# Optimization experiments

Measured on AMD Instinct MI355X. Metric: run time of the kernel, lower is better.

## Reference

```python
import jax, jax.numpy as jnp
import numpy as np

B, N, DIM, H, DH, P = 4, 4096, 256, 8, 64, 2
INNER = H * DH  # 512


def setup_inputs() -> dict:
    key = jax.random.key(0)
    ks = jax.random.split(key, 10)
    w = lambda k, shape: jax.random.normal(k, shape, dtype=jnp.float32) * 0.02
    return dict(
        x=jax.random.normal(ks[0], (B, N, DIM), dtype=jnp.float32),
        prev_x=jax.random.normal(ks[1], (B, N, DIM), dtype=jnp.float32),
        ln_q_g=jnp.ones((2 * DIM,), jnp.float32), ln_q_b=jnp.zeros((2 * DIM,), jnp.float32),
        ln_k_g=jnp.ones((DIM,), jnp.float32), ln_k_b=jnp.zeros((DIM,), jnp.float32),
        ln_v_g=jnp.ones((DIM,), jnp.float32), ln_v_b=jnp.zeros((DIM,), jnp.float32),
        Wq=w(ks[2], (2 * DIM, INNER)),            # to_q, bias=False
        Wk=w(ks[3], (DIM, INNER)), bk=jnp.zeros((INNER,), jnp.float32),
        Wv=w(ks[4], (DIM, INNER)), bv=jnp.zeros((INNER,), jnp.float32),
        Woff=w(ks[5], (H * P, INNER)),            # 1x1 conv == linear over channels
        boff=jax.random.uniform(ks[6], (H * P,), jnp.float32, -1.0, 1.0),
        Wout=w(ks[7], (DIM, INNER)), bout=jnp.zeros((DIM,), jnp.float32),
    )


def _ln(x, g, b):
    m = x.mean(-1, keepdims=True)
    v = ((x - m) ** 2).mean(-1, keepdims=True)
    return (x - m) * jax.lax.rsqrt(v + 1e-5) * g + b


def reference(x, prev_x, ln_q_g, ln_q_b, ln_k_g, ln_k_b, ln_v_g, ln_v_b,
              Wq, Wk, bk, Wv, bv, Woff, boff, Wout, bout):
    scale = DH ** -0.5
    # queries from cat(x, prev_x) along feature dim
    q = _ln(jnp.concatenate([x, prev_x], axis=-1), ln_q_g, ln_q_b) @ Wq  # (B,N,INNER)
    # learned per-head, per-point offsets (1x1 conv over channels)
    offsets = (q @ Woff.T + boff).reshape(B, N, H, P).transpose(0, 2, 3, 1)  # (B,H,P,N)
    # K/V from cat(x, prev_x) along batch dim -> KV length 2N per (b,h)
    kv = jnp.concatenate([x, prev_x], axis=0)  # (2B,N,DIM)
    k = (_ln(kv, ln_k_g, ln_k_b) @ Wk + bk).reshape(2, B, N, H, DH).transpose(1, 3, 4, 0, 2).reshape(B, H, DH, 2 * N)
    v = (_ln(kv, ln_v_g, ln_v_b) @ Wv + bv).reshape(2, B, N, H, DH).transpose(1, 3, 4, 0, 2).reshape(B, H, DH, 2 * N)
    # sampling positions: pos + offset, clamped, truncated to int (matches torch .long())
    pos = jnp.arange(N, dtype=jnp.float32)
    samp = jnp.clip(pos[None, None, None, :] + offsets, 0, 2 * N - 1).astype(jnp.int32)  # (B,H,P,N)
    idx = samp.transpose(0, 1, 3, 2)[:, :, None, :, :]  # (B,H,1,N,P)
    k_s = jnp.take_along_axis(k[:, :, :, None, :], idx, axis=-1)  # (B,H,DH,N,P)
    v_s = jnp.take_along_axis(v[:, :, :, None, :], idx, axis=-1)  # (B,H,DH,N,P)
    qh = q.reshape(B, N, H, DH).transpose(0, 2, 1, 3) * scale     # (B,H,N,DH)
    sim = jnp.einsum('bhnd,bhdnp->bhnp', qh, k_s)                  # (B,H,N,P)
    attn = jax.nn.softmax(sim, axis=-1)
    out = jnp.einsum('bhnp,bhdnp->bhnd', attn, v_s)                # (B,H,N,DH)
    out = out.transpose(0, 2, 1, 3).reshape(B, N, INNER) @ Wout.T + bout  # (B,N,DIM)
    return out, offsets
```

## Files before the change

### kernel.cpp

```cpp
#include <hip/hip_runtime.h>
#include <hip/hip_bf16.h>
#include <math.h>

#define B_    4
#define N_    4096
#define DIM_  256
#define H_    8
#define DH_   64
#define P_    2
#define INNER_ 512
#define BN_   (B_ * N_)
#define KVR_  (2 * BN_)

typedef short v8s  __attribute__((ext_vector_type(8)));
typedef short v4s  __attribute__((ext_vector_type(4)));
typedef float v4f  __attribute__((ext_vector_type(4)));

__device__ __forceinline__ short f2b(float x) {
    __hip_bfloat16 h = __float2bfloat16(x);
    return *reinterpret_cast<short*>(&h);
}
__device__ __forceinline__ float b2f(short s) {
    __hip_bfloat16 h = *reinterpret_cast<__hip_bfloat16*>(&s);
    return __bfloat162float(h);
}

__device__ __forceinline__ void async16(const void* g, void* l) {
    __builtin_amdgcn_global_load_lds(
        (const __attribute__((address_space(1))) void*)g,
        (__attribute__((address_space(3))) void*)l, 16, 0, 0);
}

__device__ __forceinline__ void storeRow(float* p, float4 f0, float4 f1, float4 f2, float4 f3) {
    ((float4*)p)[0] = f0; ((float4*)p)[1] = f1; ((float4*)p)[2] = f2; ((float4*)p)[3] = f3;
}
__device__ __forceinline__ void storeRow(__hip_bfloat16* p, float4 f0, float4 f1, float4 f2, float4 f3) {
    v8s o0, o1;
    o0[0]=f2b(f0.x); o0[1]=f2b(f0.y); o0[2]=f2b(f0.z); o0[3]=f2b(f0.w);
    o0[4]=f2b(f1.x); o0[5]=f2b(f1.y); o0[6]=f2b(f1.z); o0[7]=f2b(f1.w);
    o1[0]=f2b(f2.x); o1[1]=f2b(f2.y); o1[2]=f2b(f2.z); o1[3]=f2b(f2.w);
    o1[4]=f2b(f3.x); o1[5]=f2b(f3.y); o1[6]=f2b(f3.z); o1[7]=f2b(f3.w);
    ((v8s*)p)[0] = o0; ((v8s*)p)[1] = o1;
}

__global__ __launch_bounds__(256) void prep_all(
    const float* __restrict__ Wq, const float* __restrict__ gq, const float* __restrict__ betaq,
    const float* __restrict__ Wk, const float* __restrict__ gk, const float* __restrict__ betak,
    const float* __restrict__ bk,
    const float* __restrict__ Wv, const float* __restrict__ gv, const float* __restrict__ betav,
    const float* __restrict__ bv,
    const float* __restrict__ Woff, const float* __restrict__ Wout,
    short* __restrict__ Wq2t, float* __restrict__ bq2,
    short* __restrict__ Wkvt, float* __restrict__ bkv,
    float* __restrict__ Wcomb, float* __restrict__ braw, short* __restrict__ Woutb) {
    __shared__ float sm[272];
    const int bid = blockIdx.x, t = threadIdx.x;

    if (bid < 1536) {
        const float *W, *g, *beta, *bias_in;
        short* Wt; float* b2; int K, n; float scale;
        if (bid < 512)       { W=Wq; g=gq; beta=betaq; bias_in=nullptr; Wt=Wq2t; b2=bq2; K=512; n=bid;        scale=0.125f; }
        else if (bid < 1024) { W=Wk; g=gk; beta=betak; bias_in=bk; Wt=Wkvt;           b2=bkv;       K=256; n=bid-512;  scale=1.f; }
        else                 { W=Wv; g=gv; beta=betav; bias_in=bv; Wt=Wkvt+512*256;   b2=bkv+512;   K=256; n=bid-1024; scale=1.f; }
        float partial = 0.f;
        for (int k = t; k < K; k += 256) {
            float w = W[k * 512 + n];
            Wt[(size_t)n * K + k] = f2b(scale * g[k] * w);
            partial += beta[k] * w;
        }
        sm[t] = partial;
        __syncthreads();
        for (int s = 128; s > 0; s >>= 1) {
            if (t < s) sm[t] += sm[t + s];
            __syncthreads();
        }
        if (t == 0) b2[n] = scale * ((bias_in ? bias_in[n] : 0.f) + sm[0]);
    } else if (bid < 2048) {
        const int k = bid - 1536;
        const int hp = t & 15, jg = t >> 4;
        float p = 0.f;
        for (int j = jg; j < INNER_; j += 16)
            p += Wq[k * INNER_ + j] * Woff[hp * INNER_ + j];
        sm[jg * 17 + hp] = p;
        __syncthreads();
        if (t < 16) {
            float s = 0.f;
            for (int i = 0; i < 16; i++) s += sm[i * 17 + t];
            Wcomb[k * 16 + t] = gq[k] * s;
            braw[k * 16 + t]  = betaq[k] * s;
        }
    } else {
        const int i0 = (bid - 2048) * 1024 + t * 4;
        float4 f = *(const float4*)(Wout + i0);
        v4s o;
        o[0] = f2b(f.x); o[1] = f2b(f.y); o[2] = f2b(f.z); o[3] = f2b(f.w);
        *(v4s*)(Woutb + i0) = o;
    }
}

__global__ void bcomb_sum(const float* __restrict__ braw, const float* __restrict__ boff,
                          float* __restrict__ bcomb) {
    __shared__ float sm[272];
    int t = threadIdx.x;
    int hp = t & 15, kg = t >> 4;
    float p = 0.f;
    for (int k = kg; k < 512; k += 16) p += braw[k * 16 + hp];
    sm[kg * 17 + hp] = p;
    __syncthreads();
    if (t < 16) {
        float s = 0.f;
        for (int i = 0; i < 16; i++) s += sm[i * 17 + t];
        bcomb[t] = s + boff[t];
    }
}

__global__ __launch_bounds__(256) void norm_fused_kernel(
    const float* __restrict__ x, const float* __restrict__ p,
    const float* __restrict__ Wcomb, const float* __restrict__ bcomb,
    short* __restrict__ Aq, short* __restrict__ Akv,
    float* __restrict__ out_off, int* __restrict__ idx) {
    const int lane = threadIdx.x & 63;
    const int wv   = threadIdx.x >> 6;
    const int m0   = (blockIdx.x * 4 + wv) * 4;
    const int k8   = lane * 8;

    float4 w[8][4];
#pragma unroll
    for (int i = 0; i < 8; i++) {
        const float4* wr = (const float4*)(Wcomb + (size_t)(k8 + i) * 16);
#pragma unroll
        for (int j = 0; j < 4; j++) w[i][j] = wr[j];
    }
    const float bc = bcomb[lane & 15];

    const float* srcb = (lane < 32) ? (x + k8) : (p + k8 - DIM_);

    float4 u0 = ((const float4*)(srcb + (size_t)m0 * DIM_))[0];
    float4 u1 = ((const float4*)(srcb + (size_t)m0 * DIM_))[1];

#pragma unroll
    for (int r = 0; r < 4; r++) {
        const int m = m0 + r;
        float4 n0, n1;
        if (r < 3) {
            n0 = ((const float4*)(srcb + (size_t)(m + 1) * DIM_))[0];
            n1 = ((const float4*)(srcb + (size_t)(m + 1) * DIM_))[1];
        }
        float uv[8] = { u0.x, u0.y, u0.z, u0.w, u1.x, u1.y, u1.z, u1.w };

        float s = 0.f, q2 = 0.f;
#pragma unroll
        for (int i = 0; i < 8; i++) { s += uv[i]; q2 += uv[i] * uv[i]; }
#pragma unroll
        for (int d = 1; d <= 16; d <<= 1) {
            s  += __shfl_xor(s, d);
            q2 += __shfl_xor(q2, d);
        }
        float mean_h = s * (1.f / 256.f);
        float var_h  = q2 * (1.f / 256.f) - mean_h * mean_h;
        float rstd_h = rsqrtf(var_h + 1e-5f);
        float sf  = s  + __shfl_xor(s, 32);
        float q2f = q2 + __shfl_xor(q2, 32);
        float mean_q = sf * (1.f / 512.f);
        float var_q  = q2f * (1.f / 512.f) - mean_q * mean_q;
        float rstd_q = rsqrtf(var_q + 1e-5f);

        v8s okv;
#pragma unroll
        for (int i = 0; i < 8; i++) okv[i] = f2b((uv[i] - mean_h) * rstd_h);
        short* akvdst = Akv + ((lane < 32) ? ((size_t)m * DIM_ + k8)
                                           : ((size_t)(BN_ + m) * DIM_ + k8 - DIM_));
        *(v8s*)akvdst = okv;

        float nv[8];
        v8s oq;
#pragma unroll
        for (int i = 0; i < 8; i++) { nv[i] = (uv[i] - mean_q) * rstd_q; oq[i] = f2b(nv[i]); }
        *(v8s*)(Aq + (size_t)m * INNER_ + k8) = oq;

        float acc[16];
#pragma unroll
        for (int h = 0; h < 16; h++) acc[h] = 0.f;
#pragma unroll
        for (int i = 0; i < 8; i++) {
            float nvi = nv[i];
            acc[0]  += nvi * w[i][0].x;  acc[1]  += nvi * w[i][0].y;
            acc[2]  += nvi * w[i][0].z;  acc[3]  += nvi * w[i][0].w;
            acc[4]  += nvi * w[i][1].x;  acc[5]  += nvi * w[i][1].y;
            acc[6]  += nvi * w[i][1].z;  acc[7]  += nvi * w[i][1].w;
            acc[8]  += nvi * w[i][2].x;  acc[9]  += nvi * w[i][2].y;
            acc[10] += nvi * w[i][2].z;  acc[11] += nvi * w[i][2].w;
            acc[12] += nvi * w[i][3].x;  acc[13] += nvi * w[i][3].y;
            acc[14] += nvi * w[i][3].z;  acc[15] += nvi * w[i][3].w;
        }
        float a8[8];
#pragma unroll
        for (int j = 0; j < 8; j++) {
            float lo = acc[2 * j] + __shfl_xor(acc[2 * j], 1);
            float hi = acc[2 * j + 1] + __shfl_xor(acc[2 * j + 1], 1);
            a8[j] = (lane & 1) ? hi : lo;
        }
        float a4[4];
#pragma unroll
        for (int j = 0; j < 4; j++) {
            float lo = a8[2 * j] + __shfl_xor(a8[2 * j], 2);
            float hi = a8[2 * j + 1] + __shfl_xor(a8[2 * j + 1], 2);
            a4[j] = (lane & 2) ? hi : lo;
        }
        float a2[2];
#pragma unroll
        for (int j = 0; j < 2; j++) {
            float lo = a4[2 * j] + __shfl_xor(a4[2 * j], 4);
            float hi = a4[2 * j + 1] + __shfl_xor(a4[2 * j + 1], 4);
            a2[j] = (lane & 4) ? hi : lo;
        }
        float l1 = a2[0] + __shfl_xor(a2[0], 8);
        float h1 = a2[1] + __shfl_xor(a2[1], 8);
        float a1 = (lane & 8) ? h1 : l1;
        a1 += __shfl_xor(a1, 16);
        a1 += __shfl_xor(a1, 32);

        if (lane < 16) {
            float off = a1 + bc;
            int b = m >> 12, n = m & (N_ - 1);
            int h = lane >> 1, pp = lane & 1;
            out_off[(size_t)((b * H_ + h) * P_ + pp) * N_ + n] = off;
            float f = fminf(fmaxf((float)n + off, 0.f), (float)(2 * N_ - 1));
            idx[((size_t)(b * H_ + h) * N_ + n) * P_ + pp] = (int)f;
        }
        u0 = n0; u1 = n1;
    }
}

template <typename OT>
__device__ __forceinline__ void gemm_body(
    short* smem, const short* __restrict__ A, const short* __restrict__ Bt,
    const float* __restrict__ bias, OT* __restrict__ C, int N, int K, int nx, int lin) {
    short* As = smem;
    short* Bs = smem + 128 * 64;
    const int tid  = threadIdx.x;
    const int lane = tid & 63, w = tid >> 6;
    const int wr = w >> 1, wc = w & 1;
    const int lm = lane & 15, g = lane >> 4;

    const int x8 = lin & 7, t = lin >> 3;
    const int bx = t % nx, by = (t / nx) * 8 + x8;
    const int row0 = by * 128, col0 = bx * 128;

    const short* pa[4];
    const short* pb[4];
#pragma unroll
    for (int r = 0; r < 4; r++) {
        int s   = tid + 256 * r;
        int row = s >> 3, kcs = s & 7;
        int kg  = kcs ^ (row & 7);
        pa[r] = A  + (size_t)(row0 + row) * K + kg * 8;
        pb[r] = Bt + (size_t)(col0 + row) * K + kg * 8;
    }

    v4f acc[4][4];
#pragma unroll
    for (int i = 0; i < 4; i++)
#pragma unroll
        for (int j = 0; j < 4; j++) acc[i][j] = (v4f){0.f, 0.f, 0.f, 0.f};

    for (int k0 = 0; k0 < K; k0 += 64) {
        __syncthreads();
#pragma unroll
        for (int r = 0; r < 4; r++) {
            int s = tid + 256 * r;
            async16(pa[r] + k0, (char*)As + s * 16);
            async16(pb[r] + k0, (char*)Bs + s * 16);
        }
        __syncthreads();
#pragma unroll
        for (int ks = 0; ks < 2; ks++) {
            v8s af[4], bf[4];
#pragma unroll
            for (int i = 0; i < 4; i++) {
                int m   = wr * 64 + i * 16 + lm;
                int sch = m * 8 + ((ks * 4 + g) ^ (m & 7));
                af[i] = *(const v8s*)(As + sch * 8);
            }
#pragma unroll
            for (int j = 0; j < 4; j++) {
                int n   = wc * 64 + j * 16 + lm;
                int sch = n * 8 + ((ks * 4 + g) ^ (n & 7));
                bf[j] = *(const v8s*)(Bs + sch * 8);
            }
#pragma unroll
            for (int i = 0; i < 4; i++)
#pragma unroll
                for (int j = 0; j < 4; j++)
                    acc[i][j] = __builtin_amdgcn_mfma_f32_16x16x32_bf16(af[i], bf[j], acc[i][j], 0, 0, 0);
        }
    }

#pragma unroll
    for (int j = 0; j < 4; j++) {
        int gc = col0 + wc * 64 + j * 16 + lm;
        float bj = bias ? bias[gc] : 0.f;
#pragma unroll
        for (int i = 0; i < 4; i++)
#pragma unroll
            for (int r = 0; r < 4; r++) acc[i][j][r] += bj;
    }

    __syncthreads();
    float* ep = (float*)smem + w * (16 * 68);
#pragma unroll
    for (int i = 0; i < 4; i++) {
#pragma unroll
        for (int j = 0; j < 4; j++)
#pragma unroll
            for (int r = 0; r < 4; r++)
                ep[(g * 4 + r) * 68 + j * 16 + lm] = acc[i][j][r];
        asm volatile("s_waitcnt lgkmcnt(0)" ::: "memory");
        int rr = lane >> 2, cb = (lane & 3) * 16;
        float4 f0 = *(float4*)(ep + rr * 68 + cb + 0);
        float4 f1 = *(float4*)(ep + rr * 68 + cb + 4);
        float4 f2 = *(float4*)(ep + rr * 68 + cb + 8);
        float4 f3 = *(float4*)(ep + rr * 68 + cb + 12);
        asm volatile("s_waitcnt lgkmcnt(0)" ::: "memory");
        int grow = row0 + wr * 64 + i * 16 + rr;
        int gcol = col0 + wc * 64 + cb;
        storeRow(&C[(size_t)grow * N + gcol], f0, f1, f2, f3);
    }
}

#define ATILE_ (256 * 64)

__global__ __launch_bounds__(512, 2) void gemm_qkv_256(
    const short* __restrict__ Aqp, const short* __restrict__ Wq2t,
    const float* __restrict__ bq2, __hip_bfloat16* __restrict__ qb,
    const short* __restrict__ Akvp, const short* __restrict__ Wkvt,
    const float* __restrict__ bkv, __hip_bfloat16* __restrict__ kvproj) {
    __shared__ short smem[4 * ATILE_];

    const short* A; const short* Bt; const float* bias; __hip_bfloat16* C;
    int N, K, NT, nxs, nwg, lin;
    if ((int)blockIdx.x < 128) {
        A = Aqp;  Bt = Wq2t; bias = bq2; C = qb;
        N = 512;  K = 512; NT = 8; nxs = 1; nwg = 128; lin = blockIdx.x;
    } else {
        A = Akvp; Bt = Wkvt; bias = bkv; C = kvproj;
        N = 1024; K = 256; NT = 4; nxs = 2; nwg = 512; lin = blockIdx.x - 128;
    }

    const int tid  = threadIdx.x;
    const int lane = tid & 63, w = tid >> 6;
    const int wr = w >> 2, wc = w & 3;
    const int lm = lane & 15, g = lane >> 4;

    const int wg = (lin & 7) * (nwg >> 3) + (lin >> 3);
    const int bx = wg & ((1 << nxs) - 1), by = wg >> nxs;
    const int row0 = by << 8, col0 = bx << 8;

    short* As0 = smem;
    short* Bs0 = smem + 2 * ATILE_;

    const int kg = ((tid & 7) ^ ((tid >> 3) & 7)) << 3;
    const short* gA = A  + (size_t)(row0 + (tid >> 3)) * K + kg;
    const short* gB = Bt + (size_t)(col0 + (tid >> 3)) * K + kg;

    auto stageA = [&](int buf, int k0) {
        char* lp = (char*)(As0 + buf * ATILE_);
#pragma unroll
        for (int r = 0; r < 4; r++)
            async16(gA + (size_t)r * 64 * K + k0, lp + r * 8192 + tid * 16);
    };
    auto stageB = [&](int buf, int k0) {
        char* lp = (char*)(Bs0 + buf * ATILE_);
#pragma unroll
        for (int r = 0; r < 4; r++)
            async16(gB + (size_t)r * 64 * K + k0, lp + r * 8192 + tid * 16);
    };

    v4f acc[8][4];
#pragma unroll
    for (int i = 0; i < 8; i++)
#pragma unroll
        for (int j = 0; j < 4; j++) acc[i][j] = (v4f){0.f, 0.f, 0.f, 0.f};

    float bj[4];
#pragma unroll
    for (int jj = 0; jj < 4; jj++) bj[jj] = bias[col0 + wc * 64 + jj * 16 + lm];

    v8s aLo[4][2], aHi[4][2], bF[4][2];

    auto RD_A = [&](const short* base, int half, v8s (*dst)[2]) {
#pragma unroll
        for (int i = 0; i < 4; i++) {
            const int m = wr * 128 + half * 64 + i * 16 + lm;
#pragma unroll
            for (int ks = 0; ks < 2; ks++)
                dst[i][ks] = *(const v8s*)(base + m * 64 + (((ks << 2) | g) ^ (m & 7)) * 8);
        }
    };
    auto RD_B = [&](const short* base) {
#pragma unroll
        for (int j = 0; j < 4; j++) {
            const int n = wc * 64 + j * 16 + lm;
#pragma unroll
            for (int ks = 0; ks < 2; ks++)
                bF[j][ks] = *(const v8s*)(base + n * 64 + (((ks << 2) | g) ^ (n & 7)) * 8);
        }
    };
    auto MFMA_H = [&](int half, v8s (*af)[2]) {
        __builtin_amdgcn_s_setprio(1);
#pragma unroll
        for (int i = 0; i < 4; i++)
#pragma unroll
            for (int j = 0; j < 4; j++) {
                acc[half*4+i][j] = __builtin_amdgcn_mfma_f32_16x16x32_bf16(af[i][0], bF[j][0], acc[half*4+i][j], 0, 0, 0);
                acc[half*4+i][j] = __builtin_amdgcn_mfma_f32_16x16x32_bf16(af[i][1], bF[j][1], acc[half*4+i][j], 0, 0, 0);
            }
        __builtin_amdgcn_s_setprio(0);
    };

    stageB(0, 0); stageA(0, 0);
    stageB(1, 64); stageA(1, 64);
    asm volatile("s_waitcnt vmcnt(8)" ::: "memory");
    __builtin_amdgcn_s_barrier();
    asm volatile("" ::: "memory");

    for (int T = 0; T < NT; ++T) {
        const int cur = T & 1;
        const short* as = As0 + cur * ATILE_;
        const short* bs = Bs0 + cur * ATILE_;
        const bool s2 = (T + 2 < NT);
        const int k2 = (T + 2) << 6;

        RD_B(bs);
        RD_A(as, 0, aLo);
        asm volatile("s_waitcnt lgkmcnt(0)" ::: "memory");
        __builtin_amdgcn_s_barrier();
        if (s2) stageB(cur, k2);
        MFMA_H(0, aLo);
        RD_A(as, 1, aHi);
        asm volatile("s_waitcnt lgkmcnt(0)" ::: "memory");
        __builtin_amdgcn_s_barrier();
        if (s2) stageA(cur, k2);
        MFMA_H(1, aHi);
        if (s2)              asm volatile("s_waitcnt vmcnt(8)" ::: "memory");
        else if (T + 1 < NT) asm volatile("s_waitcnt vmcnt(0)" ::: "memory");
        __builtin_amdgcn_s_barrier();
        asm volatile("" ::: "memory");
    }

    float* ep = (float*)smem + w * (16 * 68);
#pragma unroll
    for (int ii = 0; ii < 8; ii++) {
#pragma unroll
        for (int jj = 0; jj < 4; jj++)
#pragma unroll
            for (int r = 0; r < 4; r++)
                ep[(g * 4 + r) * 68 + jj * 16 + lm] = acc[ii][jj][r] + bj[jj];
        asm volatile("s_waitcnt lgkmcnt(0)" ::: "memory");
        const int rr = lane >> 2, cb = (lane & 3) * 16;
        float4 f0 = *(float4*)(ep + rr * 68 + cb + 0);
        float4 f1 = *(float4*)(ep + rr * 68 + cb + 4);
        float4 f2 = *(float4*)(ep + rr * 68 + cb + 8);
        float4 f3 = *(float4*)(ep + rr * 68 + cb + 12);
        asm volatile("s_waitcnt lgkmcnt(0)" ::: "memory");
        const int grow = row0 + wr * 128 + ii * 16 + rr;
        const int gcol = col0 + wc * 64 + cb;
        storeRow(&C[(size_t)grow * N + gcol], f0, f1, f2, f3);
    }
}

__global__ __launch_bounds__(256) void gemm_out(
    const short* __restrict__ A, const short* __restrict__ Bt,
    const float* __restrict__ bias, float* __restrict__ C) {
    __shared__ short smem[2 * 128 * 64];
    const int lin = blockIdx.y * gridDim.x + blockIdx.x;
    gemm_body<float>(smem, A, Bt, bias, C, 256, 512, 2, lin);
}

__global__ __launch_bounds__(256) void attn_kernel(
    const short* __restrict__ qb, const short* __restrict__ kvproj,
    const int* __restrict__ idx, short* __restrict__ attnout) {
    const int lane = threadIdx.x & 63;
    const int wv   = threadIdx.x >> 6;
    const int s    = lane >> 4, c = lane & 15;
    const int n = blockIdx.x * 16 + wv * 4 + s;
    const int h = blockIdx.y, b = blockIdx.z;
    const int m = b * N_ + n;

    v4s qv = *(const v4s*)(qb + (size_t)m * INNER_ + h * DH_ + c * 4);

    const int* ip = idx + ((size_t)(b * H_ + h) * N_ + n) * P_;
    int j0 = ip[0], j1 = ip[1];
    int r0 = b * N_ + j0 + ((j0 >= N_) ? (BN_ - N_) : 0);
    int r1 = b * N_ + j1 + ((j1 >= N_) ? (BN_ - N_) : 0);
    const short* k0p = kvproj + (size_t)r0 * 1024 + h * DH_ + c * 4;
    const short* k1p = kvproj + (size_t)r1 * 1024 + h * DH_ + c * 4;
    v4s k0 = *(const v4s*)k0p, v0 = *(const v4s*)(k0p + 512);
    v4s k1 = *(const v4s*)k1p, v1 = *(const v4s*)(k1p + 512);

    float q0 = b2f(qv[0]), q1 = b2f(qv[1]), q2 = b2f(qv[2]), q3 = b2f(qv[3]);
    float s0 = q0 * b2f(k0[0]) + q1 * b2f(k0[1]) + q2 * b2f(k0[2]) + q3 * b2f(k0[3]);
    float s1 = q0 * b2f(k1[0]) + q1 * b2f(k1[1]) + q2 * b2f(k1[2]) + q3 * b2f(k1[3]);
#pragma unroll
    for (int d = 1; d <= 8; d <<= 1) {
        s0 += __shfl_xor(s0, d);
        s1 += __shfl_xor(s1, d);
    }
    float mx = fmaxf(s0, s1);
    float e0 = __expf(s0 - mx), e1 = __expf(s1 - mx);
    float inv = 1.f / (e0 + e1);
    v4s o;
#pragma unroll
    for (int i = 0; i < 4; i++)
        o[i] = f2b((e0 * b2f(v0[i]) + e1 * b2f(v1[i])) * inv);
    *(v4s*)(attnout + (size_t)m * INNER_ + h * DH_ + c * 4) = o;
}

extern "C" void kernel_launch(void* const* d_in, const int* in_sizes, int n_in,
                              void* d_out, int out_size, void* d_ws, size_t ws_size,
                              hipStream_t stream) {
    (void)in_sizes; (void)n_in; (void)out_size; (void)ws_size;

    const float* x      = (const float*)d_in[0];
    const float* prevx  = (const float*)d_in[1];
    const float* ln_q_g = (const float*)d_in[2];
    const float* ln_q_b = (const float*)d_in[3];
    const float* ln_k_g = (const float*)d_in[4];
    const float* ln_k_b = (const float*)d_in[5];
    const float* ln_v_g = (const float*)d_in[6];
    const float* ln_v_b = (const float*)d_in[7];
    const float* Wq     = (const float*)d_in[8];
    const float* Wk     = (const float*)d_in[9];
    const float* bk     = (const float*)d_in[10];
    const float* Wv     = (const float*)d_in[11];
    const float* bv     = (const float*)d_in[12];
    const float* Woff   = (const float*)d_in[13];
    const float* boff   = (const float*)d_in[14];
    const float* Wout   = (const float*)d_in[15];
    const float* bout   = (const float*)d_in[16];

    char* cur = (char*)d_ws;
    auto alloc = [&](size_t bytes) { char* p = cur; cur += (bytes + 255) & ~(size_t)255; return p; };
    short* Aq      = (short*)alloc((size_t)BN_ * INNER_ * 2);
    short* Akv     = (short*)alloc((size_t)KVR_ * DIM_ * 2);
    short* qb      = (short*)alloc((size_t)BN_ * INNER_ * 2);
    short* kvproj  = (short*)alloc((size_t)KVR_ * 1024 * 2);
    short* attnout = (short*)alloc((size_t)BN_ * INNER_ * 2);
    short* Wq2t    = (short*)alloc(512 * 512 * 2);
    short* Wkvt    = (short*)alloc(1024 * 256 * 2);
    short* Woutb   = (short*)alloc(256 * 512 * 2);
    float* bq2     = (float*)alloc(512 * 4);
    float* bkv     = (float*)alloc(1024 * 4);
    float* Wcomb   = (float*)alloc(512 * 16 * 4);
    float* braw    = (float*)alloc(512 * 16 * 4);
    float* bcomb   = (float*)alloc(16 * 4);
    int*   idxb    = (int*)alloc((size_t)BN_ * 16 * 4);

    float* out_main = (float*)d_out;
    float* out_off  = out_main + (size_t)BN_ * DIM_;

    prep_all<<<2176, 256, 0, stream>>>(Wq, ln_q_g, ln_q_b,
                                       Wk, ln_k_g, ln_k_b, bk,
                                       Wv, ln_v_g, ln_v_b, bv,
                                       Woff, Wout,
                                       Wq2t, bq2, Wkvt, bkv, Wcomb, braw, Woutb);
    bcomb_sum<<<1, 256, 0, stream>>>(braw, boff, bcomb);

    norm_fused_kernel<<<BN_ / 16, 256, 0, stream>>>(x, prevx, Wcomb, bcomb,
                                                    Aq, Akv, out_off, idxb);

    gemm_qkv_256<<<640, 512, 0, stream>>>(Aq, Wq2t, bq2, (__hip_bfloat16*)qb,
                                          Akv, Wkvt, bkv, (__hip_bfloat16*)kvproj);

    dim3 ga(N_ / 16, H_, B_);
    attn_kernel<<<ga, 256, 0, stream>>>(qb, kvproj, idxb, attnout);

    gemm_out<<<dim3(2, 128), 256, 0, stream>>>(attnout, Woutb, bout, out_main);
}
```

Before: 216.4 us.

## Store Q/K/V head-major and fold bias reduction into norm kernel

The QKV GEMM epilogue now writes Q, K and V in a head-major layout ([h][row][64]), with V in a separate plane. This makes the attention kernel's per-head gathers touch contiguous 128-byte rows instead of strided 2KB rows. The separate single-block bcomb_sum launch is removed. Each norm block now recomputes the 16 offset biases redundantly from braw, which saves a launch but adds per-block reduction work.

```diff
diff --git a/kernel.cpp b/kernel.cpp
--- a/kernel.cpp
+++ b/kernel.cpp
@@ -11,6 +11,7 @@
 #define INNER_ 512
 #define BN_   (B_ * N_)
 #define KVR_  (2 * BN_)
+#define VOFF_ ((size_t)H_ * KVR_ * DH_)
 
 typedef short v8s  __attribute__((ext_vector_type(8)));
 typedef short v4s  __attribute__((ext_vector_type(4)));
@@ -34,7 +35,7 @@
 __device__ __forceinline__ void storeRow(float* p, float4 f0, float4 f1, float4 f2, float4 f3) {
     ((float4*)p)[0] = f0; ((float4*)p)[1] = f1; ((float4*)p)[2] = f2; ((float4*)p)[3] = f3;
 }
-__device__ __forceinline__ void storeRow(__hip_bfloat16* p, float4 f0, float4 f1, float4 f2, float4 f3) {
+__device__ __forceinline__ void storeRowS(short* p, float4 f0, float4 f1, float4 f2, float4 f3) {
     v8s o0, o1;
     o0[0]=f2b(f0.x); o0[1]=f2b(f0.y); o0[2]=f2b(f0.z); o0[3]=f2b(f0.w);
     o0[4]=f2b(f1.x); o0[5]=f2b(f1.y); o0[6]=f2b(f1.z); o0[7]=f2b(f1.w);
@@ -98,32 +99,35 @@
     }
 }
 
-__global__ void bcomb_sum(const float* __restrict__ braw, const float* __restrict__ boff,
-                          float* __restrict__ bcomb) {
-    __shared__ float sm[272];
-    int t = threadIdx.x;
-    int hp = t & 15, kg = t >> 4;
-    float p = 0.f;
-    for (int k = kg; k < 512; k += 16) p += braw[k * 16 + hp];
-    sm[kg * 17 + hp] = p;
-    __syncthreads();
-    if (t < 16) {
-        float s = 0.f;
-        for (int i = 0; i < 16; i++) s += sm[i * 17 + t];
-        bcomb[t] = s + boff[t];
-    }
-}
-
 __global__ __launch_bounds__(256) void norm_fused_kernel(
     const float* __restrict__ x, const float* __restrict__ p,
-    const float* __restrict__ Wcomb, const float* __restrict__ bcomb,
+    const float* __restrict__ Wcomb, const float* __restrict__ braw,
+    const float* __restrict__ boff,
     short* __restrict__ Aq, short* __restrict__ Akv,
     float* __restrict__ out_off, int* __restrict__ idx) {
+    __shared__ float smr[272];
+    const int t    = threadIdx.x;
     const int lane = threadIdx.x & 63;
     const int wv   = threadIdx.x >> 6;
     const int m0   = (blockIdx.x * 4 + wv) * 4;
     const int k8   = lane * 8;
 
+    {
+        const int hp = t & 15, kg = t >> 4;
+        float pp = 0.f;
+        for (int k = kg; k < 512; k += 16) pp += braw[k * 16 + hp];
+        smr[kg * 17 + hp] = pp;
+    }
+    __syncthreads();
+    if (t < 16) {
+        float s = 0.f;
+#pragma unroll
+        for (int i = 0; i < 16; i++) s += smr[i * 17 + t];
+        smr[256 + t] = s + boff[t];
+    }
+    __syncthreads();
+    const float bc = smr[256 + (lane & 15)];
+
     float4 w[8][4];
 #pragma unroll
     for (int i = 0; i < 8; i++) {
@@ -131,7 +135,6 @@
 #pragma unroll
         for (int j = 0; j < 4; j++) w[i][j] = wr[j];
     }
-    const float bc = bcomb[lane & 15];
 
     const float* srcb = (lane < 32) ? (x + k8) : (p + k8 - DIM_);
 
@@ -332,19 +335,20 @@
 
 __global__ __launch_bounds__(512, 2) void gemm_qkv_256(
     const short* __restrict__ Aqp, const short* __restrict__ Wq2t,
-    const float* __restrict__ bq2, __hip_bfloat16* __restrict__ qb,
+    const float* __restrict__ bq2, short* __restrict__ qbh,
     const short* __restrict__ Akvp, const short* __restrict__ Wkvt,
-    const float* __restrict__ bkv, __hip_bfloat16* __restrict__ kvproj) {
+    const float* __restrict__ bkv, short* __restrict__ khv) {
     __shared__ short smem[4 * ATILE_];
 
-    const short* A; const short* Bt; const float* bias; __hip_bfloat16* C;
-    int N, K, NT, nxs, nwg, lin;
+    const short* A; const short* Bt; const float* bias; short* C;
+    int K, NT, nxs, nwg, lin;
+    bool isQ;
     if ((int)blockIdx.x < 128) {
-        A = Aqp;  Bt = Wq2t; bias = bq2; C = qb;
-        N = 512;  K = 512; NT = 8; nxs = 1; nwg = 128; lin = blockIdx.x;
+        A = Aqp;  Bt = Wq2t; bias = bq2; C = qbh;
+        K = 512; NT = 8; nxs = 1; nwg = 128; lin = blockIdx.x; isQ = true;
     } else {
-        A = Akvp; Bt = Wkvt; bias = bkv; C = kvproj;
-        N = 1024; K = 256; NT = 4; nxs = 2; nwg = 512; lin = blockIdx.x - 128;
+        A = Akvp; Bt = Wkvt; bias = bkv; C = khv;
+        K = 256; NT = 4; nxs = 2; nwg = 512; lin = blockIdx.x - 128; isQ = false;
     }
 
     const int tid  = threadIdx.x;
@@ -465,7 +469,16 @@
         asm volatile("s_waitcnt lgkmcnt(0)" ::: "memory");
         const int grow = row0 + wr * 128 + ii * 16 + rr;
         const int gcol = col0 + wc * 64 + cb;
-        storeRow(&C[(size_t)grow * N + gcol], f0, f1, f2, f3);
+        short* dst;
+        if (isQ) {
+            const int h = gcol >> 6;
+            dst = C + ((size_t)h * BN_ + grow) * DH_ + (gcol & 63);
+        } else {
+            const size_t base = (gcol < 512) ? 0 : VOFF_;
+            const int h = (gcol >> 6) & 7;
+            dst = C + base + ((size_t)h * KVR_ + grow) * DH_ + (gcol & 63);
+        }
+        storeRowS(dst, f0, f1, f2, f3);
     }
 }
 
@@ -478,7 +491,7 @@
 }
 
 __global__ __launch_bounds__(256) void attn_kernel(
-    const short* __restrict__ qb, const short* __restrict__ kvproj,
+    const short* __restrict__ qbh, const short* __restrict__ khv,
     const int* __restrict__ idx, short* __restrict__ attnout) {
     const int lane = threadIdx.x & 63;
     const int wv   = threadIdx.x >> 6;
@@ -487,16 +500,16 @@
     const int h = blockIdx.y, b = blockIdx.z;
     const int m = b * N_ + n;
 
-    v4s qv = *(const v4s*)(qb + (size_t)m * INNER_ + h * DH_ + c * 4);
+    v4s qv = *(const v4s*)(qbh + ((size_t)h * BN_ + m) * DH_ + c * 4);
 
     const int* ip = idx + ((size_t)(b * H_ + h) * N_ + n) * P_;
     int j0 = ip[0], j1 = ip[1];
     int r0 = b * N_ + j0 + ((j0 >= N_) ? (BN_ - N_) : 0);
     int r1 = b * N_ + j1 + ((j1 >= N_) ? (BN_ - N_) : 0);
-    const short* k0p = kvproj + (size_t)r0 * 1024 + h * DH_ + c * 4;
-    const short* k1p = kvproj + (size_t)r1 * 1024 + h * DH_ + c * 4;
-    v4s k0 = *(const v4s*)k0p, v0 = *(const v4s*)(k0p + 512);
-    v4s k1 = *(const v4s*)k1p, v1 = *(const v4s*)(k1p + 512);
+    const short* k0p = khv + ((size_t)h * KVR_ + r0) * DH_ + c * 4;
+    const short* k1p = khv + ((size_t)h * KVR_ + r1) * DH_ + c * 4;
+    v4s k0 = *(const v4s*)k0p, v0 = *(const v4s*)(k0p + VOFF_);
+    v4s k1 = *(const v4s*)k1p, v1 = *(const v4s*)(k1p + VOFF_);
 
     float q0 = b2f(qv[0]), q1 = b2f(qv[1]), q2 = b2f(qv[2]), q3 = b2f(qv[3]);
     float s0 = q0 * b2f(k0[0]) + q1 * b2f(k0[1]) + q2 * b2f(k0[2]) + q3 * b2f(k0[3]);
@@ -543,8 +556,8 @@
     auto alloc = [&](size_t bytes) { char* p = cur; cur += (bytes + 255) & ~(size_t)255; return p; };
     short* Aq      = (short*)alloc((size_t)BN_ * INNER_ * 2);
     short* Akv     = (short*)alloc((size_t)KVR_ * DIM_ * 2);
-    short* qb      = (short*)alloc((size_t)BN_ * INNER_ * 2);
-    short* kvproj  = (short*)alloc((size_t)KVR_ * 1024 * 2);
+    short* qbh     = (short*)alloc((size_t)BN_ * INNER_ * 2);
+    short* khv     = (short*)alloc((size_t)KVR_ * 1024 * 2);
     short* attnout = (short*)alloc((size_t)BN_ * INNER_ * 2);
     short* Wq2t    = (short*)alloc(512 * 512 * 2);
     short* Wkvt    = (short*)alloc(1024 * 256 * 2);
@@ -553,7 +566,6 @@
     float* bkv     = (float*)alloc(1024 * 4);
     float* Wcomb   = (float*)alloc(512 * 16 * 4);
     float* braw    = (float*)alloc(512 * 16 * 4);
-    float* bcomb   = (float*)alloc(16 * 4);
     int*   idxb    = (int*)alloc((size_t)BN_ * 16 * 4);
 
     float* out_main = (float*)d_out;
@@ -564,16 +576,15 @@
                                        Wv, ln_v_g, ln_v_b, bv,
                                        Woff, Wout,
                                        Wq2t, bq2, Wkvt, bkv, Wcomb, braw, Woutb);
-    bcomb_sum<<<1, 256, 0, stream>>>(braw, boff, bcomb);
-
-    norm_fused_kernel<<<BN_ / 16, 256, 0, stream>>>(x, prevx, Wcomb, bcomb,
+
+    norm_fused_kernel<<<BN_ / 16, 256, 0, stream>>>(x, prevx, Wcomb, braw, boff,
                                                     Aq, Akv, out_off, idxb);
 
-    gemm_qkv_256<<<640, 512, 0, stream>>>(Aq, Wq2t, bq2, (__hip_bfloat16*)qb,
-                                          Akv, Wkvt, bkv, (__hip_bfloat16*)kvproj);
+    gemm_qkv_256<<<640, 512, 0, stream>>>(Aq, Wq2t, bq2, qbh,
+                                          Akv, Wkvt, bkv, khv);
 
     dim3 ga(N_ / 16, H_, B_);
-    attn_kernel<<<ga, 256, 0, stream>>>(qb, kvproj, idxb, attnout);
+    attn_kernel<<<ga, 256, 0, stream>>>(qbh, khv, idxb, attnout);
 
     gemm_out<<<dim3(2, 128), 256, 0, stream>>>(attnout, Woutb, bout, out_main);
 }
```

New measurement: 220.9 us. +2.1%, slower.
